# Kernel optimization log

Hardware: AMD Instinct MI355X
Metric: run time of the kernel (lower is better)

## Reference

```python
import jax, jax.numpy as jnp
import numpy as np

D_MODEL = 1024
D_STATE = 128
D_CONV = 4
EXPAND = 2
HEADDIM = 64
NGROUPS = 1
CHUNK = 256
D_INNER = EXPAND * D_MODEL
D_SSM = D_INNER
NHEADS = D_SSM // HEADDIM
CONV_DIM = D_SSM + 2 * NGROUPS * D_STATE
D_IN_PROJ = 2 * D_INNER + 2 * NGROUPS * D_STATE + NHEADS
D_OUT = 1024
EPS = 1e-5
B_SZ = 2
SEQ = 4096


def setup_inputs() -> dict:
    key = jax.random.key(0)
    ks = jax.random.split(key, 8)
    inputs = jax.random.normal(ks[0], (B_SZ, SEQ, D_MODEL), jnp.float32)
    W_in = jax.random.normal(ks[1], (D_IN_PROJ, D_MODEL), jnp.float32) / np.sqrt(D_MODEL)
    conv_w = jax.random.normal(ks[2], (CONV_DIM, D_CONV), jnp.float32) / np.sqrt(D_CONV)
    conv_b = jnp.zeros((CONV_DIM,), jnp.float32)
    # dt_bias = inverse-softplus of dt sampled log-uniform in [dt_min, dt_max]
    dt = jnp.exp(jax.random.uniform(ks[3], (NHEADS,)) * (np.log(0.1) - np.log(0.001)) + np.log(0.001))
    dt_bias = dt + jnp.log(-jnp.expm1(-dt))
    A_log = jnp.log(jax.random.uniform(ks[4], (NHEADS,), minval=1.0, maxval=16.0))
    D = jnp.ones((NHEADS,), jnp.float32)
    norm_w = jnp.ones((D_SSM,), jnp.float32)
    W_out = jax.random.normal(ks[5], (D_OUT, D_INNER), jnp.float32) / np.sqrt(D_INNER)
    return dict(inputs=inputs, W_in=W_in, conv_w=conv_w, conv_b=conv_b,
                dt_bias=dt_bias, A_log=A_log, D=D, norm_w=norm_w, W_out=W_out)


def _ssd(xd, dA, Bm, Cm):
    # Chunked SSD scan (mamba_chunk_scan_combined math).
    # xd: [b,nc,c,h,p] = x * dt ; dA: [b,h,nc,c] = dt * A ; Bm/Cm: [b,nc,c,n]
    cs = jnp.cumsum(dA, axis=-1)                                    # [b,h,nc,c]
    c = dA.shape[-1]
    mask = jnp.tril(jnp.ones((c, c), bool))
    L = jnp.where(mask, jnp.exp(cs[..., :, None] - cs[..., None, :]), 0.0)  # [b,h,nc,c,c]
    Y_diag = jnp.einsum('bzln,bzsn,bhzls,bzshp->bzlhp', Cm, Bm, L, xd)
    decay_states = jnp.exp(cs[..., -1:] - cs)                        # [b,h,nc,c]
    states = jnp.einsum('bzln,bhzl,bzlhp->bzhpn', Bm, decay_states, xd)  # [b,nc,h,p,n]
    chunk_decay = jnp.exp(cs[..., -1])                               # [b,h,nc]

    def step(carry, inp):
        st, cd = inp
        return carry * cd[..., None, None] + st, carry

    init = jnp.zeros(states.shape[:1] + states.shape[2:], xd.dtype)  # [b,h,p,n]
    _, prev = jax.lax.scan(step, init, (jnp.moveaxis(states, 1, 0), jnp.moveaxis(chunk_decay, 2, 0)))
    prev = jnp.moveaxis(prev, 0, 1)                                  # [b,nc,h,p,n]
    Y_off = jnp.einsum('bzln,bhzl,bzhpn->bzlhp', Cm, jnp.exp(cs), prev)
    return Y_diag + Y_off


def reference(inputs, W_in, conv_w, conv_b, dt_bias, A_log, D, norm_w, W_out):
    b, l, _ = inputs.shape
    zxbcdt = inputs @ W_in.T                                         # [b,l,4384]
    z = zxbcdt[..., :D_SSM]
    xBC = zxbcdt[..., D_SSM:D_SSM + CONV_DIM]
    dt = zxbcdt[..., D_SSM + CONV_DIM:]                              # [b,l,h]
    # depthwise causal conv1d + silu
    xp = jnp.pad(xBC, ((0, 0), (D_CONV - 1, 0), (0, 0)))
    conv = sum(xp[:, k:k + l, :] * conv_w[:, k] for k in range(D_CONV)) + conv_b
    xBC = jax.nn.silu(conv)
    x = xBC[..., :D_SSM]
    Bc = xBC[..., D_SSM:D_SSM + D_STATE]
    Cc = xBC[..., D_SSM + D_STATE:]
    A = -jnp.exp(A_log)                                              # [h]
    dtp = jax.nn.softplus(dt + dt_bias)                              # [b,l,h]
    nc = l // CHUNK
    x4 = x.reshape(b, l, NHEADS, HEADDIM)
    xd = (x4 * dtp[..., None]).reshape(b, nc, CHUNK, NHEADS, HEADDIM)
    dA = jnp.transpose((dtp * A).reshape(b, nc, CHUNK, NHEADS), (0, 3, 1, 2))  # [b,h,nc,c]
    Bm = Bc.reshape(b, nc, CHUNK, D_STATE)
    Cm = Cc.reshape(b, nc, CHUNK, D_STATE)
    y = _ssd(xd, dA, Bm, Cm).reshape(b, l, NHEADS, HEADDIM)
    y = y + D[None, None, :, None] * x4                              # D skip on raw x
    y = y.reshape(b, l, D_SSM)
    # gated RMSNorm (norm_before_gate=False): norm(y * silu(z)) * w
    t = y * jax.nn.silu(z)
    yn = t * jax.lax.rsqrt(jnp.mean(t * t, axis=-1, keepdims=True) + EPS) * norm_w
    return yn @ W_out.T
```

## Files before the change

kernel.cpp:

```cpp
#include <hip/hip_runtime.h>
#include <hip/hip_bf16.h>
#include <math.h>

#define B_SZ     2
#define SEQ      4096
#define DMODEL   1024
#define DSTATE   128
#define HEADDIM  64
#define CHUNK    256
#define DINNER   2048
#define DSSM     2048
#define NHEADS   32
#define CONVDIM  2304
#define DOUTSZ   1024
#define NC       16
#define EPSF     1e-5f

typedef __hip_bfloat16 bf16;
typedef __attribute__((ext_vector_type(8))) short bf16x8;
typedef __attribute__((ext_vector_type(4))) float f32x4;

__device__ __forceinline__ float siluf(float x) { return x / (1.0f + expf(-x)); }

__device__ __forceinline__ float bfu(unsigned short u) {
    union { unsigned int i; float f; } c; c.i = ((unsigned int)u) << 16; return c.f;
}
__device__ __forceinline__ unsigned short f2bf(float f) {
    union { float f; unsigned int u; } c; c.f = f;
    unsigned int u = c.u;
    return (unsigned short)((u + 0x7FFFu + ((u >> 16) & 1u)) >> 16);
}

__device__ __forceinline__ void gload16(const void* g, void* l) {
    typedef __attribute__((address_space(1))) const unsigned int GU;
    typedef __attribute__((address_space(3))) unsigned int LU;
    __builtin_amdgcn_global_load_lds((GU*)g, (LU*)l, 16, 0, 0);
}

__global__ __launch_bounds__(256)
void cast_f32_bf16(const float* __restrict__ src, unsigned short* __restrict__ dst)
{
    const long long i = ((long long)blockIdx.x * 256 + threadIdx.x) * 8;
    float4 a = *(const float4*)(src + i);
    float4 b = *(const float4*)(src + i + 4);
    bf16x8 o;
    o[0] = (short)f2bf(a.x); o[1] = (short)f2bf(a.y);
    o[2] = (short)f2bf(a.z); o[3] = (short)f2bf(a.w);
    o[4] = (short)f2bf(b.x); o[5] = (short)f2bf(b.y);
    o[6] = (short)f2bf(b.z); o[7] = (short)f2bf(b.w);
    *(bf16x8*)(dst + i) = o;
}

template<bool SPLIT, typename TC>
__global__ __launch_bounds__(512)
void gemm256_nt(const short* __restrict__ A, const short* __restrict__ B,
                TC* __restrict__ C0, TC* __restrict__ C1, int M, int N, int K)
{
    const int nwg = gridDim.x * gridDim.y;
    const int orig = blockIdx.y * gridDim.x + blockIdx.x;
    const int q = nwg >> 3, r = nwg & 7;
    const int xcd = orig & 7, rest = orig >> 3;
    const int wgid = (xcd < r ? xcd * (q + 1) : r * (q + 1) + (xcd - r) * q) + rest;
    const int bx = wgid % gridDim.x;
    const int by = wgid / gridDim.x;

    __shared__ short As0[256 * 32];
    __shared__ short As1[256 * 32];
    __shared__ short Bs0[256 * 32];
    __shared__ short Bs1[256 * 32];

    const int tid  = threadIdx.x;
    const int lane = tid & 63;
    const int wid  = tid >> 6;
    const int wr = (wid >> 2) * 128;
    const int wc = (wid & 3) * 64;
    const int frow = lane & 15;
    const int fk   = lane >> 4;
    const int m0 = by * 256;
    const int n0 = bx * 256;

    const int s0 = tid, s1 = 512 + tid;
    const int r0s = s0 >> 2, c0s = (s0 & 3) ^ ((s0 >> 3) & 3);
    const int r1s = s1 >> 2, c1s = (s1 & 3) ^ ((s1 >> 3) & 3);
    const short* Ag0 = A + (long long)(m0 + r0s) * K + c0s * 8;
    const short* Ag1 = A + (long long)(m0 + r1s) * K + c1s * 8;
    const short* Bg0 = B + (long long)(n0 + r0s) * K + c0s * 8;
    const short* Bg1 = B + (long long)(n0 + r1s) * K + c1s * 8;

    short* A0w0 = &As0[(wid * 64) * 8];        short* A0w1 = &As0[(512 + wid * 64) * 8];
    short* A1w0 = &As1[(wid * 64) * 8];        short* A1w1 = &As1[(512 + wid * 64) * 8];
    short* B0w0 = &Bs0[(wid * 64) * 8];        short* B0w1 = &Bs0[(512 + wid * 64) * 8];
    short* B1w0 = &Bs1[(wid * 64) * 8];        short* B1w1 = &Bs1[(512 + wid * 64) * 8];

    const int swz = (fk ^ ((frow >> 1) & 3)) * 8;

    f32x4 acc[8][4];
    #pragma unroll
    for (int i = 0; i < 8; ++i)
        #pragma unroll
        for (int j = 0; j < 4; ++j) acc[i][j] = (f32x4)(0.0f);

    const int NT = K / 32;
    gload16(Ag0, A0w0); gload16(Ag1, A0w1);
    gload16(Bg0, B0w0); gload16(Bg1, B0w1);
    __syncthreads();

    int cur = 0;
    for (int t = 0; t < NT; ++t) {
        if (t + 1 < NT) {
            const int k = (t + 1) * 32;
            gload16(Ag0 + k, cur ? A0w0 : A1w0);
            gload16(Ag1 + k, cur ? A0w1 : A1w1);
            gload16(Bg0 + k, cur ? B0w0 : B1w0);
            gload16(Bg1 + k, cur ? B0w1 : B1w1);
        }
        const short* Asc = cur ? As1 : As0;
        const short* Bsc = cur ? Bs1 : Bs0;
        bf16x8 a[8], b[4];
        #pragma unroll
        for (int fm = 0; fm < 8; ++fm)
            a[fm] = *(const bf16x8*)&Asc[(wr + fm * 16 + frow) * 32 + swz];
        #pragma unroll
        for (int fn = 0; fn < 4; ++fn)
            b[fn] = *(const bf16x8*)&Bsc[(wc + fn * 16 + frow) * 32 + swz];
        #pragma unroll
        for (int fm = 0; fm < 8; ++fm)
            #pragma unroll
            for (int fn = 0; fn < 4; ++fn)
                acc[fm][fn] = __builtin_amdgcn_mfma_f32_16x16x32_bf16(
                    a[fm], b[fn], acc[fm][fn], 0, 0, 0);
        __syncthreads();
        cur ^= 1;
    }

    const int crow = (lane >> 4) * 4;
    const int ccol = lane & 15;
    #pragma unroll
    for (int fm = 0; fm < 8; ++fm) {
        #pragma unroll
        for (int j = 0; j < 4; ++j) {
            long long row = m0 + wr + fm * 16 + crow + j;
            #pragma unroll
            for (int fn = 0; fn < 4; ++fn) {
                int col = n0 + wc + fn * 16 + ccol;
                float v = acc[fm][fn][j];
                if constexpr (SPLIT) {
                    if (col < DSSM)
                        C0[row * DSSM + col] = (TC)f2bf(v);
                    else
                        C1[row * CONVDIM + (col - DSSM)] = (TC)f2bf(v);
                } else {
                    if constexpr (sizeof(TC) == 2) C0[row * N + col] = (TC)f2bf(v);
                    else                           C0[row * N + col] = v;
                }
            }
        }
    }
}

#define G8_DECLS()                                                                \
    __shared__ short As0[128 * 32];                                               \
    __shared__ short As1[128 * 32];                                               \
    __shared__ short As2[128 * 32];                                               \
    __shared__ short Bs0[128 * 32];                                               \
    __shared__ short Bs1[128 * 32];                                               \
    __shared__ short Bs2[128 * 32];                                               \
    const int tid  = threadIdx.x;                                                 \
    const int lane = tid & 63;                                                    \
    const int wid  = tid >> 6;                                                    \
    const int wr = (wid >> 2) * 64;                                               \
    const int wc = (wid & 3) * 32;                                                \
    const int srow = tid & 127;                                                   \
    const int skg  = tid >> 7;                                                    \
    short* AsW0 = &As0[(wid * 64) * 8];                                           \
    short* AsW1 = &As1[(wid * 64) * 8];                                           \
    short* AsW2 = &As2[(wid * 64) * 8];                                           \
    short* BsW0 = &Bs0[(wid * 64) * 8];                                           \
    short* BsW1 = &Bs1[(wid * 64) * 8];                                           \
    short* BsW2 = &Bs2[(wid * 64) * 8];                                           \
    const int frow = lane & 15;                                                   \
    const int fk   = lane >> 4;

#define G8_PIPE(K_)                                                               \
    {                                                                             \
        const int NT = (K_) / 32;                                                 \
        gload16(Ag + 0 * 32, AsW0); gload16(Bg + 0 * 32, BsW0);                   \
        gload16(Ag + 1 * 32, AsW1); gload16(Bg + 1 * 32, BsW1);                   \
        gload16(Ag + 2 * 32, AsW2); gload16(Bg + 2 * 32, BsW2);                   \
        asm volatile("s_waitcnt vmcnt(4)" ::: "memory");                          \
        __builtin_amdgcn_sched_barrier(0);                                        \
        __builtin_amdgcn_s_barrier();                                             \
        for (int t = 0; t < NT; ++t) {                                            \
            const int cur = t % 3;                                                \
            const short* Asc = cur == 0 ? As0 : (cur == 1 ? As1 : As2);           \
            const short* Bsc = cur == 0 ? Bs0 : (cur == 1 ? Bs1 : Bs2);           \
            bf16x8 a[4], b[2];                                                    \
            _Pragma("unroll")                                                     \
            for (int fm = 0; fm < 4; ++fm)                                        \
                a[fm] = *(const bf16x8*)&Asc[(fk * 128 + wr + fm * 16 + frow) * 8]; \
            _Pragma("unroll")                                                     \
            for (int fn = 0; fn < 2; ++fn)                                        \
                b[fn] = *(const bf16x8*)&Bsc[(fk * 128 + wc + fn * 16 + frow) * 8]; \
            _Pragma("unroll")                                                     \
            for (int fm = 0; fm < 4; ++fm)                                        \
                _Pragma("unroll")                                                 \
                for (int fn = 0; fn < 2; ++fn)                                    \
                    acc[fm][fn] = __builtin_amdgcn_mfma_f32_16x16x32_bf16(        \
                        a[fm], b[fn], acc[fm][fn], 0, 0, 0);                      \
            __builtin_amdgcn_s_barrier();                                         \
            if (t + 3 < NT) {                                                     \
                short* stA = cur == 0 ? AsW0 : (cur == 1 ? AsW1 : AsW2);          \
                short* stB = cur == 0 ? BsW0 : (cur == 1 ? BsW1 : BsW2);          \
                gload16(Ag + (t + 3) * 32, stA);                                  \
                gload16(Bg + (t + 3) * 32, stB);                                  \
                asm volatile("s_waitcnt vmcnt(4)" ::: "memory");                  \
            } else if (t + 2 < NT) {                                              \
                asm volatile("s_waitcnt vmcnt(2)" ::: "memory");                  \
            } else if (t + 1 < NT) {                                              \
                asm volatile("s_waitcnt vmcnt(0)" ::: "memory");                  \
            }                                                                     \
            __builtin_amdgcn_sched_barrier(0);                                    \
            __builtin_amdgcn_s_barrier();                                         \
        }                                                                         \
    }

template<typename TC>
__global__ __launch_bounds__(512)
void gemm_mfma_nt(const short* __restrict__ A, const short* __restrict__ B,
                  TC* __restrict__ C, int M, int N, int K,
                  long long sA, long long sB, long long sC)
{
    A += (long long)blockIdx.z * sA;
    B += (long long)blockIdx.z * sB;
    C += (long long)blockIdx.z * sC;

    const int nwg = gridDim.x * gridDim.y;
    const int orig = blockIdx.y * gridDim.x + blockIdx.x;
    const int q = nwg >> 3, r = nwg & 7;
    const int xcd = orig & 7, rest = orig >> 3;
    const int wgid = (xcd < r ? xcd * (q + 1) : r * (q + 1) + (xcd - r) * q) + rest;
    const int bx = wgid % gridDim.x;
    const int by = wgid / gridDim.x;

    G8_DECLS()

    const int m0 = by * 128;
    const int n0 = bx * 128;
    const short* Ag = A + (long long)(m0 + srow) * K + skg * 8;
    const short* Bg = B + (long long)(n0 + srow) * K + skg * 8;

    f32x4 acc[4][2];
    #pragma unroll
    for (int i = 0; i < 4; ++i) { acc[i][0] = (f32x4)(0.f); acc[i][1] = (f32x4)(0.f); }

    G8_PIPE(K)

    const int crow = (lane >> 4) * 4;
    const int ccol = lane & 15;
    #pragma unroll
    for (int fm = 0; fm < 4; ++fm) {
        #pragma unroll
        for (int j = 0; j < 4; ++j) {
            long long row = m0 + wr + fm * 16 + crow + j;
            TC* cp = C + row * N + n0 + wc + ccol;
            #pragma unroll
            for (int fn = 0; fn < 2; ++fn) {
                float v = acc[fm][fn][j];
                if constexpr (sizeof(TC) == 2) cp[fn * 16] = (TC)f2bf(v);
                else                           cp[fn * 16] = v;
            }
        }
    }
}

__global__ __launch_bounds__(256)
void dt_gemm_tiled(const float* __restrict__ inp, const float* __restrict__ Wdt,
                   float* __restrict__ dtraw)
{
    const int tid  = threadIdx.x;
    const int row0 = blockIdx.x * 32;
    const int hh   = (tid & 15) * 2;
    const int rr   = (tid >> 4) * 2;

    __shared__ float Wl[32][130];
    __shared__ float Il[32][130];

    float a00 = 0.f, a01 = 0.f, a10 = 0.f, a11 = 0.f;

    for (int k0 = 0; k0 < DMODEL; k0 += 128) {
        #pragma unroll
        for (int it = 0; it < 16; ++it) {
            int idx = it * 256 + tid;
            int r = idx >> 7, c = idx & 127;
            Wl[r][c] = Wdt[(long long)r * DMODEL + k0 + c];
            Il[r][c] = inp[(long long)(row0 + r) * DMODEL + k0 + c];
        }
        __syncthreads();
        #pragma unroll
        for (int kk = 0; kk < 128; kk += 4) {
            float4 w0 = *(const float4*)&Wl[hh][kk];
            float4 w1 = *(const float4*)&Wl[hh + 1][kk];
            float4 i0 = *(const float4*)&Il[rr][kk];
            float4 i1 = *(const float4*)&Il[rr + 1][kk];
            a00 += i0.x * w0.x + i0.y * w0.y + i0.z * w0.z + i0.w * w0.w;
            a01 += i0.x * w1.x + i0.y * w1.y + i0.z * w1.z + i0.w * w1.w;
            a10 += i1.x * w0.x + i1.y * w0.y + i1.z * w0.z + i1.w * w0.w;
            a11 += i1.x * w1.x + i1.y * w1.y + i1.z * w1.z + i1.w * w1.w;
        }
        __syncthreads();
    }
    dtraw[(long long)(row0 + rr) * NHEADS + hh]         = a00;
    dtraw[(long long)(row0 + rr) * NHEADS + hh + 1]     = a01;
    dtraw[(long long)(row0 + rr + 1) * NHEADS + hh]     = a10;
    dtraw[(long long)(row0 + rr + 1) * NHEADS + hh + 1] = a11;
}

__global__ __launch_bounds__(256)
void conv_silu_v2(const unsigned short* __restrict__ xbc, const float* __restrict__ cw,
                  const float* __restrict__ cb,
                  unsigned short* __restrict__ xconv, unsigned short* __restrict__ Bc,
                  unsigned short* __restrict__ Cc)
{
    const int tid = threadIdx.x;
    const int c8  = (blockIdx.x * 32 + (tid & 31)) * 8;
    const int lf  = blockIdx.y * 8 + (tid >> 5);
    const int b   = lf >> 12;
    const int l   = lf & (SEQ - 1);

    float4 w[8];
    #pragma unroll
    for (int j = 0; j < 8; ++j) w[j] = *(const float4*)(cw + (c8 + j) * 4);

    float acc[8];
    {
        float4 b0 = *(const float4*)(cb + c8);
        float4 b1 = *(const float4*)(cb + c8 + 4);
        acc[0] = b0.x; acc[1] = b0.y; acc[2] = b0.z; acc[3] = b0.w;
        acc[4] = b1.x; acc[5] = b1.y; acc[6] = b1.z; acc[7] = b1.w;
    }
    #pragma unroll
    for (int k = 0; k < 4; ++k) {
        int ls = l - 3 + k;
        if (ls < 0) continue;
        const unsigned short* src = xbc + ((long long)(b * SEQ + ls)) * CONVDIM + c8;
        ushort4 v0 = *(const ushort4*)src;
        ushort4 v1 = *(const ushort4*)(src + 4);
        unsigned short tv[8] = {v0.x, v0.y, v0.z, v0.w, v1.x, v1.y, v1.z, v1.w};
        #pragma unroll
        for (int j = 0; j < 8; ++j) {
            const float* wj = (const float*)&w[j];
            acc[j] += bfu(tv[j]) * wj[k];
        }
    }
    bf16x8 o;
    #pragma unroll
    for (int j = 0; j < 8; ++j) {
        float v = acc[j];
        v = v / (1.0f + __expf(-v));
        o[j] = (short)f2bf(v);
    }
    if (c8 < DSSM)
        *(bf16x8*)(xconv + (long long)lf * DSSM + c8) = o;
    else if (c8 < DSSM + DSTATE)
        *(bf16x8*)(Bc + (long long)lf * DSTATE + (c8 - DSSM)) = o;
    else
        *(bf16x8*)(Cc + (long long)lf * DSTATE + (c8 - DSSM - DSTATE)) = o;
}

__global__ __launch_bounds__(256)
void cumsum_da(const float* __restrict__ dtraw, const float* __restrict__ dt_bias,
               const float* __restrict__ A_log, float* __restrict__ dtp,
               float* __restrict__ cs)
{
    const int bid = blockIdx.x;
    const int z = bid % NC;
    const int h = (bid / NC) % NHEADS;
    const int b = bid / (NC * NHEADS);
    const int t = threadIdx.x;

    const float Ah = -expf(A_log[h]);
    const int lg = z * CHUNK + t;
    const long long fi = ((long long)(b * SEQ) + lg) * NHEADS + h;
    float x = dtraw[fi] + dt_bias[h];
    float sp = (x > 20.f) ? x : log1pf(expf(x));
    dtp[fi] = sp;
    float v = sp * Ah;

    __shared__ float s[CHUNK];
    s[t] = v;
    __syncthreads();
    for (int off = 1; off < CHUNK; off <<= 1) {
        float add = (t >= off) ? s[t - off] : 0.f;
        __syncthreads();
        s[t] += add;
        __syncthreads();
    }
    cs[((long long)(b * NHEADS) + h) * SEQ + lg] = s[t];
}

__global__ __launch_bounds__(256)
void xdt_prep(const unsigned short* __restrict__ xconv, const float* __restrict__ dtp,
              unsigned short* __restrict__ xdT)
{
    const int st = blockIdx.x;
    const int h  = blockIdx.y;
    const int b  = blockIdx.z;
    const int tid = threadIdx.x;
    const int s0t = st * 128;

    __shared__ short T[128][66];
    __shared__ float scale[128];

    if (tid < 128) {
        int sg = s0t + tid;
        scale[tid] = dtp[((long long)(b * SEQ) + sg) * NHEADS + h];
    }
    __syncthreads();

    #pragma unroll
    for (int it = 0; it < 4; ++it) {
        int c = it * 256 + tid;
        int row = c >> 3, pc = c & 7;
        const unsigned short* src =
            xconv + ((long long)(b * SEQ) + s0t + row) * DSSM + h * 64 + pc * 8;
        ushort4 v0 = *(const ushort4*)src;
        ushort4 v1 = *(const ushort4*)(src + 4);
        float sc = scale[row];
        unsigned short tv[8] = {v0.x, v0.y, v0.z, v0.w, v1.x, v1.y, v1.z, v1.w};
        #pragma unroll
        for (int j = 0; j < 8; ++j) T[row][pc * 8 + j] = (short)f2bf(bfu(tv[j]) * sc);
    }
    __syncthreads();

    #pragma unroll
    for (int it = 0; it < 4; ++it) {
        int c = it * 256 + tid;
        int p = c >> 4, scc = c & 15;
        bf16x8 o;
        #pragma unroll
        for (int j = 0; j < 8; ++j) o[j] = T[scc * 8 + j][p];
        *(bf16x8*)(xdT + (((long long)(b * NHEADS) + h) * 64 + p) * SEQ + s0t + scc * 8) = o;
    }
}

__global__ __launch_bounds__(256)
void bt_prep(const unsigned short* __restrict__ Bc, unsigned short* __restrict__ BT)
{
    const int st = blockIdx.x;
    const int b  = blockIdx.y;
    const int tid = threadIdx.x;
    const int s0t = st * 128;

    __shared__ short T[128][130];

    #pragma unroll
    for (int it = 0; it < 8; ++it) {
        int c = it * 256 + tid;
        int row = c >> 4, nc = c & 15;
        const unsigned short* src = Bc + ((long long)(b * SEQ) + s0t + row) * DSTATE + nc * 8;
        ushort4 v0 = *(const ushort4*)src;
        ushort4 v1 = *(const ushort4*)(src + 4);
        T[row][nc * 8 + 0] = v0.x; T[row][nc * 8 + 1] = v0.y;
        T[row][nc * 8 + 2] = v0.z; T[row][nc * 8 + 3] = v0.w;
        T[row][nc * 8 + 4] = v1.x; T[row][nc * 8 + 5] = v1.y;
        T[row][nc * 8 + 6] = v1.z; T[row][nc * 8 + 7] = v1.w;
    }
    __syncthreads();

    #pragma unroll
    for (int it = 0; it < 8; ++it) {
        int c = it * 256 + tid;
        int n = c >> 4, scc = c & 15;
        bf16x8 o;
        #pragma unroll
        for (int j = 0; j < 8; ++j) o[j] = T[scc * 8 + j][n];
        *(bf16x8*)(BT + ((long long)b * DSTATE + n) * SEQ + s0t + scc * 8) = o;
    }
}

__global__ __launch_bounds__(256)
void chunk_states_mfma(const unsigned short* __restrict__ BT,
                       const unsigned short* __restrict__ xdT,
                       const float* __restrict__ cs,
                       unsigned short* __restrict__ statesbf)
{
    const int h  = blockIdx.x & 31;
    const int bz = blockIdx.x >> 5;
    const int z  = bz & (NC - 1);
    const int b  = bz >> 4;
    const int tid = threadIdx.x;
    const int lane = tid & 63;
    const int wid = tid >> 6;
    const int frow = lane & 15;
    const int fk = lane >> 4;
    const int wn = wid * 32;

    __shared__ __attribute__((aligned(16))) short Xs[4 * 64 * 8];
    __shared__ __attribute__((aligned(16))) short Bs2[4 * 128 * 8];
    __shared__ float dec[CHUNK];

    const long long csbase = ((long long)(b * NHEADS) + h) * SEQ + (long long)z * CHUNK;
    {
        float clast = cs[csbase + CHUNK - 1];
        dec[tid] = __expf(clast - cs[csbase + tid]);
    }
    __syncthreads();

    f32x4 acc[4][2];
    #pragma unroll
    for (int i = 0; i < 4; ++i) { acc[i][0] = (f32x4)(0.f); acc[i][1] = (f32x4)(0.f); }

    const unsigned short* xdbase = xdT + (((long long)(b * NHEADS) + h) * 64) * SEQ + (long long)z * CHUNK;
    const unsigned short* btbase = BT + (long long)b * DSTATE * SEQ + (long long)z * CHUNK;

    for (int l0 = 0; l0 < CHUNK; l0 += 32) {
        gload16(xdbase + (long long)lane * SEQ + l0 + wid * 8, Xs + wid * 64 * 8);
        #pragma unroll
        for (int r = 0; r < 2; ++r) {
            int sidx = r * 256 + tid;
            int n = sidx & 127, lseg = sidx >> 7;
            const unsigned short* sp = btbase + (long long)n * SEQ + l0 + lseg * 8;
            ushort4 v0 = *(const ushort4*)sp;
            ushort4 v1 = *(const ushort4*)(sp + 4);
            unsigned short tv[8] = {v0.x, v0.y, v0.z, v0.w, v1.x, v1.y, v1.z, v1.w};
            bf16x8 o;
            #pragma unroll
            for (int j = 0; j < 8; ++j)
                o[j] = (short)f2bf(bfu(tv[j]) * dec[l0 + lseg * 8 + j]);
            *(bf16x8*)&Bs2[sidx * 8] = o;
        }
        __syncthreads();
        bf16x8 a[4], bb[2];
        #pragma unroll
        for (int fm = 0; fm < 4; ++fm)
            a[fm] = *(const bf16x8*)&Xs[(fk * 64 + fm * 16 + frow) * 8];
        #pragma unroll
        for (int fn = 0; fn < 2; ++fn)
            bb[fn] = *(const bf16x8*)&Bs2[(fk * 128 + wn + fn * 16 + frow) * 8];
        #pragma unroll
        for (int fm = 0; fm < 4; ++fm)
            #pragma unroll
            for (int fn = 0; fn < 2; ++fn)
                acc[fm][fn] = __builtin_amdgcn_mfma_f32_16x16x32_bf16(
                    a[fm], bb[fn], acc[fm][fn], 0, 0, 0);
        __syncthreads();
    }

    unsigned short* st = statesbf + ((long long)(bz * NHEADS + h)) * HEADDIM * DSTATE;
    const int crow = (lane >> 4) * 4;
    const int ccol = lane & 15;
    #pragma unroll
    for (int fm = 0; fm < 4; ++fm)
        #pragma unroll
        for (int j = 0; j < 4; ++j) {
            int p = fm * 16 + crow + j;
            #pragma unroll
            for (int fn = 0; fn < 2; ++fn)
                st[p * DSTATE + wn + fn * 16 + ccol] = f2bf(acc[fm][fn][j]);
        }
}

__global__ __launch_bounds__(256)
void chunk_scan(unsigned short* __restrict__ states, const float* __restrict__ cs)
{
    int f = blockIdx.x * 256 + threadIdx.x;
    int n = f & 127;
    int p = (f >> 7) & 63;
    int h = (f >> 13) & 31;
    int b = f >> 18;

    float carry = 0.f;
    for (int z = 0; z < NC; ++z) {
        long long idx = ((((long long)(b * NC + z) * NHEADS) + h) * HEADDIM + p) * DSTATE + n;
        float st = bfu(states[idx]);
        states[idx] = f2bf(carry);
        float cd = expf(cs[((long long)(b * NHEADS) + h) * SEQ + z * CHUNK + CHUNK - 1]);
        carry = carry * cd + st;
    }
}

__global__ __launch_bounds__(256)
void y_fused(const unsigned short* __restrict__ Smat, const unsigned short* __restrict__ Cc,
             const unsigned short* __restrict__ xdT, const unsigned short* __restrict__ prevbf,
             const float* __restrict__ cs, const float* __restrict__ Dv,
             const unsigned short* __restrict__ xconv, unsigned short* __restrict__ y)
{
    const int h  = blockIdx.x & 31;
    const int bz = blockIdx.x >> 5;
    const int z  = bz & (NC - 1);
    const int b  = bz >> 4;
    const int r0 = blockIdx.y * 128;
    const int tid = threadIdx.x;
    const int lane = tid & 63;
    const int wid = tid >> 6;
    const int frow = lane & 15;
    const int fk = lane >> 4;
    const int wr = wid * 32;

    __shared__ __attribute__((aligned(16))) short Ms[4 * 128 * 8];
    __shared__ __attribute__((aligned(16))) short Xs[4 * 64 * 8];
    __shared__ float css[CHUNK];

    const long long csbase = ((long long)(b * NHEADS) + h) * SEQ + (long long)z * CHUNK;
    const long long rowbase = (long long)b * SEQ + (long long)z * CHUNK;

    css[tid] = cs[csbase + tid];
    __syncthreads();

    const int lrow = tid & 127;
    const int grow = r0 + lrow;
    const int g0   = (tid >> 7) * 2;
    const float cl = css[grow];

    f32x4 acc[2][4];
    #pragma unroll
    for (int i = 0; i < 2; ++i)
        #pragma unroll
        for (int j = 0; j < 4; ++j) acc[i][j] = (f32x4)(0.0f);

    const unsigned short* Srow = Smat + ((long long)bz * CHUNK + grow) * CHUNK;
    const unsigned short* xdbase = xdT + (((long long)(b * NHEADS) + h) * 64) * SEQ + (long long)z * CHUNK;

    for (int s0 = 0; s0 < r0 + 128; s0 += 32) {
        gload16(xdbase + (long long)lane * SEQ + s0 + wid * 8, Xs + wid * 64 * 8);
        #pragma unroll
        for (int gg = 0; gg < 2; ++gg) {
            const int g = g0 + gg;
            bf16x8 o;
            if (s0 + g * 8 <= grow) {
                const unsigned short* sp = Srow + s0 + g * 8;
                ushort4 v0 = *(const ushort4*)sp;
                ushort4 v1 = *(const ushort4*)(sp + 4);
                unsigned short tv[8] = {v0.x, v0.y, v0.z, v0.w, v1.x, v1.y, v1.z, v1.w};
                #pragma unroll
                for (int j = 0; j < 8; ++j) {
                    int sg = s0 + g * 8 + j;
                    float m = (sg <= grow) ? bfu(tv[j]) * __expf(cl - css[sg]) : 0.f;
                    o[j] = (short)f2bf(m);
                }
            } else {
                #pragma unroll
                for (int j = 0; j < 8; ++j) o[j] = 0;
            }
            *(bf16x8*)&Ms[(g * 128 + lrow) * 8] = o;
        }
        __syncthreads();
        if (s0 <= r0 + wr + 31) {
            __builtin_amdgcn_s_setprio(1);
            bf16x8 a[2], bb[4];
            #pragma unroll
            for (int fm = 0; fm < 2; ++fm)
                a[fm] = *(const bf16x8*)&Ms[(fk * 128 + wr + fm * 16 + frow) * 8];
            #pragma unroll
            for (int fn = 0; fn < 4; ++fn)
                bb[fn] = *(const bf16x8*)&Xs[(fk * 64 + fn * 16 + frow) * 8];
            #pragma unroll
            for (int fm = 0; fm < 2; ++fm)
                #pragma unroll
                for (int fn = 0; fn < 4; ++fn)
                    acc[fm][fn] = __builtin_amdgcn_mfma_f32_16x16x32_bf16(
                        a[fm], bb[fn], acc[fm][fn], 0, 0, 0);
            __builtin_amdgcn_s_setprio(0);
        }
        __syncthreads();
    }

    const float el = __expf(cl);
    const unsigned short* Crow = Cc + (rowbase + grow) * DSTATE;
    const unsigned short* pvb = prevbf + (long long)(bz * NHEADS + h) * HEADDIM * DSTATE;
    for (int n0 = 0; n0 < DSTATE; n0 += 32) {
        gload16(pvb + (long long)lane * DSTATE + n0 + wid * 8, Xs + wid * 64 * 8);
        #pragma unroll
        for (int gg = 0; gg < 2; ++gg) {
            const int g = g0 + gg;
            const unsigned short* sp = Crow + n0 + g * 8;
            ushort4 v0 = *(const ushort4*)sp;
            ushort4 v1 = *(const ushort4*)(sp + 4);
            unsigned short tv[8] = {v0.x, v0.y, v0.z, v0.w, v1.x, v1.y, v1.z, v1.w};
            bf16x8 o;
            #pragma unroll
            for (int j = 0; j < 8; ++j) o[j] = (short)f2bf(bfu(tv[j]) * el);
            *(bf16x8*)&Ms[(g * 128 + lrow) * 8] = o;
        }
        __syncthreads();
        {
            __builtin_amdgcn_s_setprio(1);
            bf16x8 a[2], bb[4];
            #pragma unroll
            for (int fm = 0; fm < 2; ++fm)
                a[fm] = *(const bf16x8*)&Ms[(fk * 128 + wr + fm * 16 + frow) * 8];
            #pragma unroll
            for (int fn = 0; fn < 4; ++fn)
                bb[fn] = *(const bf16x8*)&Xs[(fk * 64 + fn * 16 + frow) * 8];
            #pragma unroll
            for (int fm = 0; fm < 2; ++fm)
                #pragma unroll
                for (int fn = 0; fn < 4; ++fn)
                    acc[fm][fn] = __builtin_amdgcn_mfma_f32_16x16x32_bf16(
                        a[fm], bb[fn], acc[fm][fn], 0, 0, 0);
            __builtin_amdgcn_s_setprio(0);
        }
        __syncthreads();
    }

    const float Dh = Dv[h];
    const int crow = (lane >> 4) * 4;
    const int ccol = lane & 15;
    #pragma unroll
    for (int fm = 0; fm < 2; ++fm) {
        #pragma unroll
        for (int j = 0; j < 4; ++j) {
            long long row = rowbase + r0 + wr + fm * 16 + crow + j;
            const unsigned short* xr = xconv + row * DSSM + h * 64;
            unsigned short* yr = y + row * DSSM + h * 64;
            #pragma unroll
            for (int fn = 0; fn < 4; ++fn) {
                int p = fn * 16 + ccol;
                yr[p] = f2bf(acc[fm][fn][j] + Dh * bfu(xr[p]));
            }
        }
    }
}

__global__ __launch_bounds__(256)
void gated_rmsnorm(bf16* __restrict__ y, const bf16* __restrict__ z,
                   const float* __restrict__ nw)
{
    const int row = blockIdx.x;
    const int tid = threadIdx.x;
    bf16* yr = y + (long long)row * DSSM;
    const bf16* zr = z + (long long)row * DSSM;

    float t[8];
    float ss = 0.f;
    const int c0 = tid * 8;
    #pragma unroll
    for (int j = 0; j < 8; ++j) {
        float zv = __bfloat162float(zr[c0 + j]);
        float tv = __bfloat162float(yr[c0 + j]) * siluf(zv);
        t[j] = tv;
        ss += tv * tv;
    }
    #pragma unroll
    for (int off = 32; off > 0; off >>= 1) ss += __shfl_down(ss, off);
    __shared__ float red[4];
    if ((tid & 63) == 0) red[tid >> 6] = ss;
    __syncthreads();
    float tot = red[0] + red[1] + red[2] + red[3];
    float rs = rsqrtf(tot / (float)DSSM + EPSF);
    #pragma unroll
    for (int j = 0; j < 8; ++j)
        yr[c0 + j] = __float2bfloat16(t[j] * rs * nw[c0 + j]);
}

extern "C" void kernel_launch(void* const* d_in, const int* in_sizes, int n_in,
                              void* d_out, int out_size, void* d_ws, size_t ws_size,
                              hipStream_t stream)
{
    const float* inp     = (const float*)d_in[0];
    const float* W_in    = (const float*)d_in[1];
    const float* conv_w  = (const float*)d_in[2];
    const float* conv_b  = (const float*)d_in[3];
    const float* dt_bias = (const float*)d_in[4];
    const float* A_log   = (const float*)d_in[5];
    const float* Dv      = (const float*)d_in[6];
    const float* norm_w  = (const float*)d_in[7];
    const float* W_out   = (const float*)d_in[8];
    float* out = (float*)d_out;

    char* ws = (char*)d_ws;
    size_t off = 0;
    auto alloc = [&](size_t bytes) -> void* {
        void* p = (void*)(ws + off);
        off = (off + bytes + 255) & ~(size_t)255;
        return p;
    };
    const int MR = B_SZ * SEQ;

    bf16*  zb     = (bf16*) alloc((size_t)MR * DSSM * 2);
    bf16*  xbc    = (bf16*) alloc((size_t)MR * CONVDIM * 2);
    bf16*  xconv  = (bf16*) alloc((size_t)MR * DSSM * 2);
    bf16*  Bc     = (bf16*) alloc((size_t)MR * DSTATE * 2);
    bf16*  Cc     = (bf16*) alloc((size_t)MR * DSTATE * 2);
    float* dtraw  = (float*)alloc((size_t)MR * NHEADS * 4);
    float* dtp    = (float*)alloc((size_t)MR * NHEADS * 4);
    float* cs     = (float*)alloc((size_t)B_SZ * NHEADS * SEQ * 4);
    unsigned short* statesbf = (unsigned short*)
                    alloc((size_t)B_SZ * NC * NHEADS * HEADDIM * DSTATE * 2);
    unsigned short* Wob = (unsigned short*)alloc((size_t)DOUTSZ * DINNER * 2);
    unsigned short* xdT = (unsigned short*)alloc((size_t)B_SZ * NHEADS * 64 * SEQ * 2);

    bf16*  Smat = (bf16*)xbc;
    bf16*  ybuf = (bf16*)((char*)xbc + (size_t)B_SZ * NC * CHUNK * CHUNK * 2);
    unsigned short* BT   = (unsigned short*)ybuf;
    unsigned short* inpb = (unsigned short*)statesbf;
    unsigned short* Wb   = (unsigned short*)xconv;

    dim3 blk(256);
    dim3 blk512(512);

    cast_f32_bf16<<<dim3((MR * DMODEL) / (256 * 8)), blk, 0, stream>>>(inp, inpb);
    cast_f32_bf16<<<dim3((4384 * DMODEL) / (256 * 8)), blk, 0, stream>>>(W_in, Wb);
    cast_f32_bf16<<<dim3((DOUTSZ * DINNER) / (256 * 8)), blk, 0, stream>>>(W_out, Wob);

    gemm256_nt<true, unsigned short><<<dim3((DSSM + CONVDIM) / 256, MR / 256), blk512, 0, stream>>>(
        (const short*)inpb, (const short*)Wb,
        (unsigned short*)zb, (unsigned short*)xbc, MR, DSSM + CONVDIM, DMODEL);
    dt_gemm_tiled<<<dim3(MR / 32), blk, 0, stream>>>(
        inp, W_in + (size_t)(DSSM + CONVDIM) * DMODEL, dtraw);

    conv_silu_v2<<<dim3(CONVDIM / 256, MR / 8), blk, 0, stream>>>(
        (const unsigned short*)xbc, conv_w, conv_b,
        (unsigned short*)xconv, (unsigned short*)Bc, (unsigned short*)Cc);

    cumsum_da<<<dim3(B_SZ * NHEADS * NC), blk, 0, stream>>>(dtraw, dt_bias, A_log, dtp, cs);

    gemm_mfma_nt<unsigned short><<<dim3(CHUNK / 128, CHUNK / 128, B_SZ * NC), blk512, 0, stream>>>(
        (const short*)Cc, (const short*)Bc, (unsigned short*)Smat, CHUNK, CHUNK, DSTATE,
        (long long)CHUNK * DSTATE, (long long)CHUNK * DSTATE, (long long)CHUNK * CHUNK);

    xdt_prep<<<dim3(SEQ / 128, NHEADS, B_SZ), blk, 0, stream>>>(
        (const unsigned short*)xconv, dtp, xdT);

    bt_prep<<<dim3(SEQ / 128, B_SZ), blk, 0, stream>>>((const unsigned short*)Bc, BT);

    chunk_states_mfma<<<dim3(B_SZ * NC * NHEADS), blk, 0, stream>>>(BT, xdT, cs, statesbf);

    chunk_scan<<<dim3(B_SZ * NHEADS * HEADDIM * DSTATE / 256), blk, 0, stream>>>(statesbf, cs);

    y_fused<<<dim3(B_SZ * NC * NHEADS, 2), blk, 0, stream>>>(
        (const unsigned short*)Smat, (const unsigned short*)Cc, xdT, statesbf,
        cs, Dv, (const unsigned short*)xconv, (unsigned short*)ybuf);

    gated_rmsnorm<<<dim3(MR), blk, 0, stream>>>(ybuf, zb, norm_w);

    gemm256_nt<false, float><<<dim3(DOUTSZ / 256, MR / 256), blk512, 0, stream>>>(
        (const short*)ybuf, (const short*)Wob, out, nullptr, MR, DOUTSZ, DINNER);
}
```

Before: 418.6 us.

## Swizzle LDS tile layout for coalesced loads and switch out-proj to 128-tile GEMM

Changes the global-to-LDS staging in the 128-tile GEMM, chunk_states and y_fused kernels so that four consecutive threads load one row's 32-element K-slice contiguously. A row-major LDS layout with an XOR swizzle keeps the fragment reads free of bank conflicts. This is meant to make global loads more coalesced, since each thread previously fetched a separate row with a large stride. The output projection also moves from the 256-tile GEMM to the swizzled 128-tile GEMM with a larger grid, which trades per-block data reuse for more parallelism.

```diff
diff --git a/kernel.cpp b/kernel.cpp
--- a/kernel.cpp
+++ b/kernel.cpp
@@ -170,8 +170,8 @@
     const int wid  = tid >> 6;                                                    \
     const int wr = (wid >> 2) * 64;                                               \
     const int wc = (wid & 3) * 32;                                                \
-    const int srow = tid & 127;                                                   \
-    const int skg  = tid >> 7;                                                    \
+    const int srow = tid >> 2;                                                    \
+    const int schk = (tid & 3) ^ ((tid >> 3) & 3);                                \
     short* AsW0 = &As0[(wid * 64) * 8];                                           \
     short* AsW1 = &As1[(wid * 64) * 8];                                           \
     short* AsW2 = &As2[(wid * 64) * 8];                                           \
@@ -179,7 +179,8 @@
     short* BsW1 = &Bs1[(wid * 64) * 8];                                           \
     short* BsW2 = &Bs2[(wid * 64) * 8];                                           \
     const int frow = lane & 15;                                                   \
-    const int fk   = lane >> 4;
+    const int fk   = lane >> 4;                                                   \
+    const int swz  = (fk ^ ((frow >> 1) & 3)) * 8;
 
 #define G8_PIPE(K_)                                                               \
     {                                                                             \
@@ -197,10 +198,10 @@
             bf16x8 a[4], b[2];                                                    \
             _Pragma("unroll")                                                     \
             for (int fm = 0; fm < 4; ++fm)                                        \
-                a[fm] = *(const bf16x8*)&Asc[(fk * 128 + wr + fm * 16 + frow) * 8]; \
+                a[fm] = *(const bf16x8*)&Asc[(wr + fm * 16 + frow) * 32 + swz];   \
             _Pragma("unroll")                                                     \
             for (int fn = 0; fn < 2; ++fn)                                        \
-                b[fn] = *(const bf16x8*)&Bsc[(fk * 128 + wc + fn * 16 + frow) * 8]; \
+                b[fn] = *(const bf16x8*)&Bsc[(wc + fn * 16 + frow) * 32 + swz];   \
             _Pragma("unroll")                                                     \
             for (int fm = 0; fm < 4; ++fm)                                        \
                 _Pragma("unroll")                                                 \
@@ -246,8 +247,8 @@
 
     const int m0 = by * 128;
     const int n0 = bx * 128;
-    const short* Ag = A + (long long)(m0 + srow) * K + skg * 8;
-    const short* Bg = B + (long long)(n0 + srow) * K + skg * 8;
+    const short* Ag = A + (long long)(m0 + srow) * K + schk * 8;
+    const short* Bg = B + (long long)(n0 + srow) * K + schk * 8;
 
     f32x4 acc[4][2];
     #pragma unroll
@@ -494,8 +495,9 @@
     const int frow = lane & 15;
     const int fk = lane >> 4;
     const int wn = wid * 32;
-
-    __shared__ __attribute__((aligned(16))) short Xs[4 * 64 * 8];
+    const int swz = (fk ^ ((frow >> 1) & 3)) * 8;
+
+    __shared__ __attribute__((aligned(16))) short Xs[64 * 32];
     __shared__ __attribute__((aligned(16))) short Bs2[4 * 128 * 8];
     __shared__ float dec[CHUNK];
 
@@ -513,8 +515,12 @@
     const unsigned short* xdbase = xdT + (((long long)(b * NHEADS) + h) * 64) * SEQ + (long long)z * CHUNK;
     const unsigned short* btbase = BT + (long long)b * DSTATE * SEQ + (long long)z * CHUNK;
 
+    const int sp_ = tid >> 2;
+    const int sc_ = (tid & 3) ^ ((tid >> 3) & 3);
+    short* XsW = &Xs[(wid * 64) * 8];
+
     for (int l0 = 0; l0 < CHUNK; l0 += 32) {
-        gload16(xdbase + (long long)lane * SEQ + l0 + wid * 8, Xs + wid * 64 * 8);
+        gload16(xdbase + (long long)sp_ * SEQ + l0 + sc_ * 8, XsW);
         #pragma unroll
         for (int r = 0; r < 2; ++r) {
             int sidx = r * 256 + tid;
@@ -533,7 +539,7 @@
         bf16x8 a[4], bb[2];
         #pragma unroll
         for (int fm = 0; fm < 4; ++fm)
-            a[fm] = *(const bf16x8*)&Xs[(fk * 64 + fm * 16 + frow) * 8];
+            a[fm] = *(const bf16x8*)&Xs[(fm * 16 + frow) * 32 + swz];
         #pragma unroll
         for (int fn = 0; fn < 2; ++fn)
             bb[fn] = *(const bf16x8*)&Bs2[(fk * 128 + wn + fn * 16 + frow) * 8];
@@ -596,9 +602,10 @@
     const int frow = lane & 15;
     const int fk = lane >> 4;
     const int wr = wid * 32;
+    const int swz = (fk ^ ((frow >> 1) & 3)) * 8;
 
     __shared__ __attribute__((aligned(16))) short Ms[4 * 128 * 8];
-    __shared__ __attribute__((aligned(16))) short Xs[4 * 64 * 8];
+    __shared__ __attribute__((aligned(16))) short Xs[64 * 32];
     __shared__ float css[CHUNK];
 
     const long long csbase = ((long long)(b * NHEADS) + h) * SEQ + (long long)z * CHUNK;
@@ -612,6 +619,10 @@
     const int g0   = (tid >> 7) * 2;
     const float cl = css[grow];
 
+    const int sp_ = tid >> 2;
+    const int sc_ = (tid & 3) ^ ((tid >> 3) & 3);
+    short* XsW = &Xs[(wid * 64) * 8];
+
     f32x4 acc[2][4];
     #pragma unroll
     for (int i = 0; i < 2; ++i)
@@ -622,7 +633,7 @@
     const unsigned short* xdbase = xdT + (((long long)(b * NHEADS) + h) * 64) * SEQ + (long long)z * CHUNK;
 
     for (int s0 = 0; s0 < r0 + 128; s0 += 32) {
-        gload16(xdbase + (long long)lane * SEQ + s0 + wid * 8, Xs + wid * 64 * 8);
+        gload16(xdbase + (long long)sp_ * SEQ + s0 + sc_ * 8, XsW);
         #pragma unroll
         for (int gg = 0; gg < 2; ++gg) {
             const int g = g0 + gg;
@@ -653,7 +664,7 @@
                 a[fm] = *(const bf16x8*)&Ms[(fk * 128 + wr + fm * 16 + frow) * 8];
             #pragma unroll
             for (int fn = 0; fn < 4; ++fn)
-                bb[fn] = *(const bf16x8*)&Xs[(fk * 64 + fn * 16 + frow) * 8];
+                bb[fn] = *(const bf16x8*)&Xs[(fn * 16 + frow) * 32 + swz];
             #pragma unroll
             for (int fm = 0; fm < 2; ++fm)
                 #pragma unroll
@@ -669,7 +680,7 @@
     const unsigned short* Crow = Cc + (rowbase + grow) * DSTATE;
     const unsigned short* pvb = prevbf + (long long)(bz * NHEADS + h) * HEADDIM * DSTATE;
     for (int n0 = 0; n0 < DSTATE; n0 += 32) {
-        gload16(pvb + (long long)lane * DSTATE + n0 + wid * 8, Xs + wid * 64 * 8);
+        gload16(pvb + (long long)sp_ * DSTATE + n0 + sc_ * 8, XsW);
         #pragma unroll
         for (int gg = 0; gg < 2; ++gg) {
             const int g = g0 + gg;
@@ -691,7 +702,7 @@
                 a[fm] = *(const bf16x8*)&Ms[(fk * 128 + wr + fm * 16 + frow) * 8];
             #pragma unroll
             for (int fn = 0; fn < 4; ++fn)
-                bb[fn] = *(const bf16x8*)&Xs[(fk * 64 + fn * 16 + frow) * 8];
+                bb[fn] = *(const bf16x8*)&Xs[(fn * 16 + frow) * 32 + swz];
             #pragma unroll
             for (int fm = 0; fm < 2; ++fm)
                 #pragma unroll
@@ -834,6 +845,6 @@
 
     gated_rmsnorm<<<dim3(MR), blk, 0, stream>>>(ybuf, zb, norm_w);
 
-    gemm256_nt<false, float><<<dim3(DOUTSZ / 256, MR / 256), blk512, 0, stream>>>(
-        (const short*)ybuf, (const short*)Wob, out, nullptr, MR, DOUTSZ, DINNER);
-}
+    gemm_mfma_nt<float><<<dim3(DOUTSZ / 128, MR / 128), blk512, 0, stream>>>(
+        (const short*)ybuf, (const short*)Wob, out, MR, DOUTSZ, DINNER, 0, 0, 0);
+}
```

Result: faster. 401.6 us (-4.1%).
